# Kernel tuning notes

Measured on AMD Instinct MI355X. Metric: run time of the kernel, lower is better.

Reference implementation:

```python
import jax, jax.numpy as jnp
import numpy as np

N_NODES = 50000
N_EDGES = 800000
N_REL = 16
D = 64          # entity_dim == relation_dim == n_hidden
NEG_SLOPE = 0.01  # torch F.leaky_relu default


def setup_inputs() -> dict:
    key = jax.random.key(0)
    ks = jax.random.split(key, 12)
    s = 1.0 / np.sqrt(D)
    return {
        "node_ids": jnp.arange(N_NODES, dtype=jnp.int64) if jax.config.jax_enable_x64 else jnp.arange(N_NODES, dtype=jnp.int32),
        "relation_ids": jax.random.randint(ks[0], (N_EDGES,), 0, N_REL),
        "src": jax.random.randint(ks[1], (N_EDGES,), 0, N_NODES),
        "dst": jax.random.randint(ks[2], (N_EDGES,), 0, N_NODES),
        "entity_embed": jax.random.normal(ks[3], (N_NODES, D), jnp.float32) * s,
        "relation_embed": jax.random.normal(ks[4], (N_REL, D), jnp.float32) * s,
        "W0": jax.random.normal(ks[5], (N_REL, D, D), jnp.float32) * s,
        "W1": jax.random.normal(ks[6], (N_REL, D, D), jnp.float32) * s,
        "ra0": jax.random.normal(ks[7], (D, D), jnp.float32) * s,
        "rb0": jax.random.normal(ks[8], (D, D), jnp.float32) * s,
        "ra1": jax.random.normal(ks[9], (D, D), jnp.float32) * s,
        "rb1": jax.random.normal(ks[10], (D, D), jnp.float32) * s,
    }


def _edge_softmax(scores, dst, n_nodes):
    # segment softmax over edges grouped by destination node (DGL edge_softmax)
    m = jax.ops.segment_max(scores, dst, num_segments=n_nodes)  # [N]
    e = jnp.exp(scores - m[dst])                                # [E]
    z = jax.ops.segment_sum(e, dst, num_segments=n_nodes)       # [N]
    return e / z[dst]


def _kgat_layer(h, efeat, src, dst, etype, Wr, ra, rb, n_nodes):
    # transform every node under every relation once: [N, R, Dr]
    trans = jnp.einsum('nd,rde->nre', h, Wr)
    t_r = trans[src, etype]                   # W_r h_t  [E, Dr]
    h_r = trans[dst, etype]                   # W_r h_h  [E, Dr]
    att = jnp.sum(t_r * jnp.tanh(h_r + efeat), axis=1)  # [E]
    a = _edge_softmax(att, dst, n_nodes)                 # [E]
    # u_mul_e + sum: scatter-add weighted source features to dst
    h_nb = jax.ops.segment_sum(h[src] * a[:, None], dst, num_segments=n_nodes)
    # Bi residual
    out = (jax.nn.leaky_relu((h + h_nb) @ ra, NEG_SLOPE)
           + jax.nn.leaky_relu((h * h_nb) @ rb, NEG_SLOPE))
    return out


def reference(node_ids, relation_ids, src, dst, entity_embed, relation_embed,
              W0, W1, ra0, rb0, ra1, rb1):
    h = entity_embed[node_ids]                 # [N, D]
    efeat = relation_embed[relation_ids]       # [E, D]
    n_nodes = node_ids.shape[0]
    cache = [h]
    for Wr, ra, rb in ((W0, ra0, rb0), (W1, ra1, rb1)):
        h = _kgat_layer(h, efeat, src, dst, relation_ids, Wr, ra, rb, n_nodes)
        cache.append(h)
    return jnp.concatenate(cache, axis=1)      # [N, 3*D]
```

## Files before the change

### kernel.cpp

```cpp
#include <hip/hip_runtime.h>
#include <hip/hip_bf16.h>
#include <math.h>

#define NN 50000
#define NE 800000
#define NR 16
#define DD 64
#define OSTRIDE 192
#define QSTRIDE 1032

typedef __attribute__((ext_vector_type(8))) short bf16x8;
typedef __attribute__((ext_vector_type(4))) float f32x4;

__device__ inline float tanh_fast(float x) {
    return 1.f - 2.f / (__expf(2.f * x) + 1.f);
}
__device__ inline unsigned short f2bf(float f) {
    unsigned u = __float_as_uint(f);
    return (unsigned short)((u + 0x7fffu + ((u >> 16) & 1u)) >> 16);
}
__device__ inline float bf2f(unsigned short s) {
    return __uint_as_float((unsigned)s << 16);
}

__global__ void k_deg(const int* __restrict__ dst, int* __restrict__ cnt) {
    for (int e = blockIdx.x * blockDim.x + threadIdx.x; e < NE;
         e += gridDim.x * blockDim.x)
        atomicAdd(&cnt[dst[e]], 1);
}

__global__ __launch_bounds__(256) void k_scan1(const int* __restrict__ cnt,
                                               int* __restrict__ rowptr,
                                               int* __restrict__ bsum) {
    __shared__ int sh[256];
    int b = blockIdx.x, t = threadIdx.x;
    int i = b * 256 + t;
    int v = (i < NN) ? cnt[i] : 0;
    sh[t] = v;
    __syncthreads();
    #pragma unroll
    for (int o = 1; o < 256; o <<= 1) {
        int u = (t >= o) ? sh[t - o] : 0;
        __syncthreads();
        sh[t] += u;
        __syncthreads();
    }
    if (i < NN) rowptr[i] = sh[t] - v;
    if (t == 255) bsum[b] = sh[255];
}

__global__ __launch_bounds__(256) void k_scan2(int* __restrict__ bsum, int nb) {
    __shared__ int sh[256];
    int t = threadIdx.x;
    int v = (t < nb) ? bsum[t] : 0;
    sh[t] = v;
    __syncthreads();
    #pragma unroll
    for (int o = 1; o < 256; o <<= 1) {
        int u = (t >= o) ? sh[t - o] : 0;
        __syncthreads();
        sh[t] += u;
        __syncthreads();
    }
    if (t < nb) bsum[t] = sh[t] - v;
}

__global__ __launch_bounds__(256) void k_scan3(int* __restrict__ rowptr,
                                               const int* __restrict__ bsum,
                                               int* __restrict__ cursor) {
    int b = blockIdx.x, t = threadIdx.x;
    int i = b * 256 + t;
    if (i < NN) {
        int v = rowptr[i] + bsum[b];
        rowptr[i] = v;
        cursor[i] = v;
    }
    if (i == 0) rowptr[NN] = NE;
}

__global__ void k_fill(const int* __restrict__ dst, const int* __restrict__ src,
                       const int* __restrict__ rel, int* __restrict__ cursor,
                       int* __restrict__ epack) {
    for (int e = blockIdx.x * blockDim.x + threadIdx.x; e < NE;
         e += gridDim.x * blockDim.x) {
        int pos = atomicAdd(&cursor[dst[e]], 1);
        epack[pos] = src[e] | (rel[e] << 16);
    }
}

__global__ void k_copy_h0(const int* __restrict__ node_ids,
                          const float* __restrict__ ent,
                          float* __restrict__ out,
                          unsigned short* __restrict__ hbf) {
    int i = blockIdx.x * blockDim.x + threadIdx.x;
    if (i >= NN * DD) return;
    int n = i >> 6, d = i & 63;
    float v = ent[(size_t)node_ids[n] * DD + d];
    out[(size_t)n * OSTRIDE + d] = v;
    hbf[(size_t)n * DD + d] = f2bf(v);
}

__global__ void k_wprep(const float* __restrict__ W, unsigned short* __restrict__ wbf,
                        unsigned short* __restrict__ wtbf) {
    int i = blockIdx.x * blockDim.x + threadIdx.x;
    if (i >= NR * DD * DD) return;
    int r = i >> 12, rem = i & 4095, d = rem >> 6, E = rem & 63;
    unsigned short v = f2bf(W[i]);
    wbf[i] = v;
    wtbf[(r << 12) | (E << 6) | d] = v;
}

__global__ __launch_bounds__(1024) void k_fused6(const unsigned short* __restrict__ hbf,
                                                 const unsigned short* __restrict__ wbf,
                                                 const unsigned short* __restrict__ wtbf,
                                                 const float* __restrict__ relE,
                                                 const int* __restrict__ rowptr,
                                                 const int* __restrict__ epack,
                                                 float* __restrict__ h_nb) {
    __shared__ __align__(16) unsigned short q_lds[16 * QSTRIDE];
    __shared__ __align__(16) unsigned short u_lds[16][16][72];
    int n0 = blockIdx.x * 16;
    int t  = threadIdx.x;
    int w  = t >> 6, l = t & 63;
    int l15 = l & 15, lg = l >> 4;
    int r = w;

    {
        int ar = n0 + l15; if (ar >= NN) ar = NN - 1;
        const unsigned short* ap = hbf + (size_t)ar * DD + lg * 8;
        bf16x8 a0 = *(const bf16x8*)ap;
        bf16x8 a1 = *(const bf16x8*)(ap + 32);

        f32x4 acc[4];
        #pragma unroll
        for (int nt = 0; nt < 4; ++nt) acc[nt] = (f32x4){0.f, 0.f, 0.f, 0.f};
        const unsigned short* wtr = wtbf + (r << 12);
        #pragma unroll
        for (int nt = 0; nt < 4; ++nt) {
            const unsigned short* bp = wtr + (nt * 16 + l15) * DD + lg * 8;
            bf16x8 b0 = *(const bf16x8*)bp;
            bf16x8 b1 = *(const bf16x8*)(bp + 32);
            acc[nt] = __builtin_amdgcn_mfma_f32_16x16x32_bf16(a0, b0, acc[nt], 0, 0, 0);
            acc[nt] = __builtin_amdgcn_mfma_f32_16x16x32_bf16(a1, b1, acc[nt], 0, 0, 0);
        }

        #pragma unroll
        for (int nt = 0; nt < 4; ++nt) {
            int E = nt * 16 + l15;
            float er = relE[r * DD + E];
            #pragma unroll
            for (int reg = 0; reg < 4; ++reg)
                u_lds[w][lg * 4 + reg][E] = f2bf(tanh_fast(acc[nt][reg] + er));
        }
        asm volatile("s_waitcnt lgkmcnt(0)" ::: "memory");

        const unsigned short* up = &u_lds[w][l15][lg * 8];
        bf16x8 u0 = *(const bf16x8*)up;
        bf16x8 u1 = *(const bf16x8*)(up + 32);

        f32x4 q4[4];
        #pragma unroll
        for (int nt = 0; nt < 4; ++nt) q4[nt] = (f32x4){0.f, 0.f, 0.f, 0.f};
        const unsigned short* wr = wbf + (r << 12);
        #pragma unroll
        for (int nt = 0; nt < 4; ++nt) {
            const unsigned short* bp = wr + (nt * 16 + l15) * DD + lg * 8;
            bf16x8 b0 = *(const bf16x8*)bp;
            bf16x8 b1 = *(const bf16x8*)(bp + 32);
            q4[nt] = __builtin_amdgcn_mfma_f32_16x16x32_bf16(u0, b0, q4[nt], 0, 0, 0);
            q4[nt] = __builtin_amdgcn_mfma_f32_16x16x32_bf16(u1, b1, q4[nt], 0, 0, 0);
        }

        #pragma unroll
        for (int reg = 0; reg < 4; ++reg) {
            unsigned short* qp = q_lds + (lg * 4 + reg) * QSTRIDE + r * 64 + l15;
            #pragma unroll
            for (int nt = 0; nt < 4; ++nt)
                qp[nt * 16] = f2bf(q4[nt][reg]);
        }
    }
    __syncthreads();

    int n = n0 + w;
    if (n >= NN) return;
    int lane = l;
    const unsigned short* ql = q_lds + w * QSTRIDE;
    int row0 = rowptr[n], deg = rowptr[n + 1] - row0;

    float m = -__builtin_inff(), zr = 0.f, acc = 0.f;
    bool s0 = lane & 1, s1 = lane & 2, s2 = lane & 4;

    int i = 0;
    for (; i + 8 <= deg; i += 8) {
        float v[8], hv[8];
        #pragma unroll
        for (int j = 0; j < 8; ++j) {
            int p = epack[row0 + i + j];
            int s = p & 0xffff, rr = p >> 16;
            hv[j] = bf2f(hbf[(size_t)s * DD + lane]);
            v[j]  = hv[j] * bf2f(ql[rr * DD + lane]);
        }
        float x0 = s0 ? v[1] : v[0], o0 = s0 ? v[0] : v[1];
        float x1 = s0 ? v[3] : v[2], o1 = s0 ? v[2] : v[3];
        float x2 = s0 ? v[5] : v[4], o2 = s0 ? v[4] : v[5];
        float x3 = s0 ? v[7] : v[6], o3 = s0 ? v[6] : v[7];
        x0 += __shfl_xor(o0, 1, 64);
        x1 += __shfl_xor(o1, 1, 64);
        x2 += __shfl_xor(o2, 1, 64);
        x3 += __shfl_xor(o3, 1, 64);
        float y0 = s1 ? x1 : x0, p0 = s1 ? x0 : x1;
        float y1 = s1 ? x3 : x2, p1 = s1 ? x2 : x3;
        y0 += __shfl_xor(p0, 2, 64);
        y1 += __shfl_xor(p1, 2, 64);
        float sj = s2 ? y1 : y0, q0 = s2 ? y0 : y1;
        sj += __shfl_xor(q0, 4, 64);
        sj += __shfl_xor(sj, 8, 64);
        sj += __shfl_xor(sj, 16, 64);
        sj += __shfl_xor(sj, 32, 64);

        float cm = sj;
        cm = fmaxf(cm, __shfl_xor(cm, 1, 64));
        cm = fmaxf(cm, __shfl_xor(cm, 2, 64));
        cm = fmaxf(cm, __shfl_xor(cm, 4, 64));
        float mn = fmaxf(m, cm);
        float sc = __expf(m - mn);
        float wgt = __expf(sj - mn);
        float zn = wgt;
        zn += __shfl_xor(zn, 1, 64);
        zn += __shfl_xor(zn, 2, 64);
        zn += __shfl_xor(zn, 4, 64);
        zr = zr * sc + zn;
        acc *= sc;
        #pragma unroll
        for (int j = 0; j < 8; ++j)
            acc += __shfl(wgt, j, 8) * hv[j];
        m = mn;
    }
    for (; i < deg; ++i) {
        int p = epack[row0 + i];
        int s = p & 0xffff, rr = p >> 16;
        float hsv = bf2f(hbf[(size_t)s * DD + lane]);
        float v = hsv * bf2f(ql[rr * DD + lane]);
        #pragma unroll
        for (int o = 32; o; o >>= 1) v += __shfl_xor(v, o, 64);
        float mn = fmaxf(m, v);
        float sc = __expf(m - mn);
        float wgt = __expf(v - mn);
        zr  = zr * sc + wgt;
        acc = acc * sc + wgt * hsv;
        m = mn;
    }
    h_nb[(size_t)n * DD + lane] = (deg > 0) ? acc / zr : 0.f;
}

__global__ __launch_bounds__(256) void k_out2(const float* __restrict__ h_nb,
                                              const float* __restrict__ ra,
                                              const float* __restrict__ rb,
                                              float* __restrict__ out,
                                              int off_in, int off_out,
                                              unsigned short* __restrict__ hbf) {
    __shared__ __align__(16) float v1s[64][68];
    __shared__ __align__(16) float v2s[64][68];
    __shared__ __align__(16) float ws[2][64][64];
    int t = threadIdx.x;
    int n0 = blockIdx.x * 64;

    for (int i = t; i < 1024; i += 256) {
        int ni = i >> 4, c4 = (i & 15) * 4;
        int n = n0 + ni;
        float4 hv = make_float4(0.f, 0.f, 0.f, 0.f);
        float4 nb = make_float4(0.f, 0.f, 0.f, 0.f);
        if (n < NN) {
            hv = *(const float4*)&out[(size_t)n * OSTRIDE + off_in + c4];
            nb = *(const float4*)&h_nb[(size_t)n * DD + c4];
        }
        v1s[c4 + 0][ni] = hv.x + nb.x;  v2s[c4 + 0][ni] = hv.x * nb.x;
        v1s[c4 + 1][ni] = hv.y + nb.y;  v2s[c4 + 1][ni] = hv.y * nb.y;
        v1s[c4 + 2][ni] = hv.z + nb.z;  v2s[c4 + 2][ni] = hv.z * nb.z;
        v1s[c4 + 3][ni] = hv.w + nb.w;  v2s[c4 + 3][ni] = hv.w * nb.w;
    }
    for (int i = t; i < 2048; i += 256) {
        const float* base = (i < 1024) ? ra : rb;
        int rem = i & 1023;
        float4 v = *(const float4*)&base[rem * 4];
        int k = rem >> 4, c4 = (rem & 15) * 4;
        *(float4*)&ws[i >> 10][k][c4] = v;
    }
    __syncthreads();

    int nd0 = (t >> 4) * 4;
    int c0  = (t & 15) * 4;
    float a1[4][4] = {}, a2[4][4] = {};
    #pragma unroll 8
    for (int k = 0; k < 64; ++k) {
        float4 h1 = *(const float4*)&v1s[k][nd0];
        float4 h2 = *(const float4*)&v2s[k][nd0];
        float4 wa = *(const float4*)&ws[0][k][c0];
        float4 wb = *(const float4*)&ws[1][k][c0];
        float x1[4] = {h1.x, h1.y, h1.z, h1.w};
        float x2[4] = {h2.x, h2.y, h2.z, h2.w};
        #pragma unroll
        for (int i = 0; i < 4; ++i) {
            a1[i][0] += x1[i] * wa.x; a1[i][1] += x1[i] * wa.y;
            a1[i][2] += x1[i] * wa.z; a1[i][3] += x1[i] * wa.w;
            a2[i][0] += x2[i] * wb.x; a2[i][1] += x2[i] * wb.y;
            a2[i][2] += x2[i] * wb.z; a2[i][3] += x2[i] * wb.w;
        }
    }
    #pragma unroll
    for (int i = 0; i < 4; ++i) {
        int n = n0 + nd0 + i;
        if (n >= NN) continue;
        float4 o;
        float* po = (float*)&o;
        #pragma unroll
        for (int j = 0; j < 4; ++j) {
            float u1 = a1[i][j], u2 = a2[i][j];
            u1 = u1 > 0.f ? u1 : 0.01f * u1;
            u2 = u2 > 0.f ? u2 : 0.01f * u2;
            po[j] = u1 + u2;
        }
        *(float4*)&out[(size_t)n * OSTRIDE + off_out + c0] = o;
        hbf[(size_t)n * DD + c0 + 0] = f2bf(o.x);
        hbf[(size_t)n * DD + c0 + 1] = f2bf(o.y);
        hbf[(size_t)n * DD + c0 + 2] = f2bf(o.z);
        hbf[(size_t)n * DD + c0 + 3] = f2bf(o.w);
    }
}

extern "C" void kernel_launch(void* const* d_in, const int* in_sizes, int n_in,
                              void* d_out, int out_size, void* d_ws, size_t ws_size,
                              hipStream_t stream) {
    const int*   node_ids = (const int*)d_in[0];
    const int*   rel_ids  = (const int*)d_in[1];
    const int*   src      = (const int*)d_in[2];
    const int*   dst      = (const int*)d_in[3];
    const float* ent      = (const float*)d_in[4];
    const float* relE     = (const float*)d_in[5];
    const float* W[2]  = {(const float*)d_in[6], (const float*)d_in[7]};
    const float* ra[2] = {(const float*)d_in[8], (const float*)d_in[10]};
    const float* rb[2] = {(const float*)d_in[9], (const float*)d_in[11]};
    float* out = (float*)d_out;

    const size_t hnb_bytes    = (size_t)NN * DD * sizeof(float);
    const size_t hbf_bytes    = (size_t)NN * DD * sizeof(short);
    const size_t wbf_bytes    = (size_t)NR * DD * DD * sizeof(short);
    const size_t epack_bytes  = (size_t)NE * sizeof(int);
    const size_t rowptr_bytes = (size_t)(NN + 1) * sizeof(int);
    const size_t cnt_bytes    = (size_t)NN * sizeof(int);
    const int    NB_SCAN      = (NN + 255) / 256;
    const size_t bsum_bytes   = (size_t)256 * sizeof(int);

    char* p = (char*)d_ws;
    float*          h_nb   = (float*)p;          p += hnb_bytes;
    unsigned short* hbf    = (unsigned short*)p; p += hbf_bytes;
    unsigned short* wbf    = (unsigned short*)p; p += wbf_bytes;
    unsigned short* wtbf   = (unsigned short*)p; p += wbf_bytes;
    int*            epack  = (int*)p;            p += epack_bytes;
    int*            rowptr = (int*)p;            p += rowptr_bytes;
    int*            cnt    = (int*)p;            p += cnt_bytes;
    int*            bsum   = (int*)p;            p += bsum_bytes;
    (void)ws_size;

    hipMemsetAsync(cnt, 0, cnt_bytes, stream);
    k_deg  <<<1024, 256, 0, stream>>>(dst, cnt);
    k_scan1<<<NB_SCAN, 256, 0, stream>>>(cnt, rowptr, bsum);
    k_scan2<<<1, 256, 0, stream>>>(bsum, NB_SCAN);
    k_scan3<<<NB_SCAN, 256, 0, stream>>>(rowptr, bsum, cnt);
    k_fill <<<1024, 256, 0, stream>>>(dst, src, rel_ids, cnt, epack);

    k_copy_h0<<<(NN * DD + 255) / 256, 256, 0, stream>>>(node_ids, ent, out, hbf);

    for (int L = 0; L < 2; ++L) {
        int off_in = L * DD;
        int off_out = (L + 1) * DD;

        k_wprep <<<(NR * DD * DD + 255) / 256, 256, 0, stream>>>(W[L], wbf, wtbf);
        k_fused6<<<(NN + 15) / 16, 1024, 0, stream>>>(hbf, wbf, wtbf, relE,
                                                      rowptr, epack, h_nb);
        k_out2  <<<(NN + 63) / 64, 256, 0, stream>>>(h_nb, ra[L], rb[L], out,
                                                     off_in, off_out, hbf);
    }
}
```

Baseline: 458.7 us.

## Process four edges per wavefront concurrently with per-group online softmax merge

The per-node edge aggregation loop now splits the 64-lane wavefront into four 16-lane groups. Each group handles one edge at a time with 4 features per lane, loaded as vectorized uint2 reads. Each group keeps its own online-softmax max, sum and accumulators, and these are merged across groups with cross-lane shuffles at the end. This replaces the earlier 8-edge batched scheme that relied on long shuffle-reduction chains. The aim is to shorten reduction latency and widen memory loads, at the cost of masked idle lanes when the degree is not a multiple of four.

```diff
diff --git a/kernel.cpp b/kernel.cpp
--- a/kernel.cpp
+++ b/kernel.cpp
@@ -110,7 +110,7 @@
     wtbf[(r << 12) | (E << 6) | d] = v;
 }
 
-__global__ __launch_bounds__(1024) void k_fused6(const unsigned short* __restrict__ hbf,
+__global__ __launch_bounds__(1024) void k_fused7(const unsigned short* __restrict__ hbf,
                                                  const unsigned short* __restrict__ wbf,
                                                  const unsigned short* __restrict__ wtbf,
                                                  const float* __restrict__ relE,
@@ -183,74 +183,63 @@
 
     int n = n0 + w;
     if (n >= NN) return;
-    int lane = l;
     const unsigned short* ql = q_lds + w * QSTRIDE;
-    int row0 = rowptr[n], deg = rowptr[n + 1] - row0;
-
-    float m = -__builtin_inff(), zr = 0.f, acc = 0.f;
-    bool s0 = lane & 1, s1 = lane & 2, s2 = lane & 4;
-
-    int i = 0;
-    for (; i + 8 <= deg; i += 8) {
-        float v[8], hv[8];
-        #pragma unroll
-        for (int j = 0; j < 8; ++j) {
-            int p = epack[row0 + i + j];
-            int s = p & 0xffff, rr = p >> 16;
-            hv[j] = bf2f(hbf[(size_t)s * DD + lane]);
-            v[j]  = hv[j] * bf2f(ql[rr * DD + lane]);
-        }
-        float x0 = s0 ? v[1] : v[0], o0 = s0 ? v[0] : v[1];
-        float x1 = s0 ? v[3] : v[2], o1 = s0 ? v[2] : v[3];
-        float x2 = s0 ? v[5] : v[4], o2 = s0 ? v[4] : v[5];
-        float x3 = s0 ? v[7] : v[6], o3 = s0 ? v[6] : v[7];
-        x0 += __shfl_xor(o0, 1, 64);
-        x1 += __shfl_xor(o1, 1, 64);
-        x2 += __shfl_xor(o2, 1, 64);
-        x3 += __shfl_xor(o3, 1, 64);
-        float y0 = s1 ? x1 : x0, p0 = s1 ? x0 : x1;
-        float y1 = s1 ? x3 : x2, p1 = s1 ? x2 : x3;
-        y0 += __shfl_xor(p0, 2, 64);
-        y1 += __shfl_xor(p1, 2, 64);
-        float sj = s2 ? y1 : y0, q0 = s2 ? y0 : y1;
-        sj += __shfl_xor(q0, 4, 64);
-        sj += __shfl_xor(sj, 8, 64);
-        sj += __shfl_xor(sj, 16, 64);
-        sj += __shfl_xor(sj, 32, 64);
-
-        float cm = sj;
-        cm = fmaxf(cm, __shfl_xor(cm, 1, 64));
-        cm = fmaxf(cm, __shfl_xor(cm, 2, 64));
-        cm = fmaxf(cm, __shfl_xor(cm, 4, 64));
-        float mn = fmaxf(m, cm);
-        float sc = __expf(m - mn);
-        float wgt = __expf(sj - mn);
-        float zn = wgt;
-        zn += __shfl_xor(zn, 1, 64);
-        zn += __shfl_xor(zn, 2, 64);
-        zn += __shfl_xor(zn, 4, 64);
-        zr = zr * sc + zn;
-        acc *= sc;
-        #pragma unroll
-        for (int j = 0; j < 8; ++j)
-            acc += __shfl(wgt, j, 8) * hv[j];
-        m = mn;
-    }
-    for (; i < deg; ++i) {
-        int p = epack[row0 + i];
+    int row0 = rowptr[n], row1 = rowptr[n + 1];
+    int deg = row1 - row0;
+    int g = lg;
+
+    const float NEGBIG = -1e30f;
+    float m = NEGBIG, zr = 0.f;
+    float a0 = 0.f, a1 = 0.f, a2 = 0.f, a3 = 0.f;
+
+    int steps = (deg + 3) >> 2;
+    for (int k = 0; k < steps; ++k) {
+        int idx = row0 + (k << 2) + g;
+        bool ok = idx < row1;
+        int p = epack[ok ? idx : row0];
         int s = p & 0xffff, rr = p >> 16;
-        float hsv = bf2f(hbf[(size_t)s * DD + lane]);
-        float v = hsv * bf2f(ql[rr * DD + lane]);
-        #pragma unroll
-        for (int o = 32; o; o >>= 1) v += __shfl_xor(v, o, 64);
+        uint2 hu = *(const uint2*)(hbf + ((size_t)s << 6) + (l15 << 2));
+        uint2 qu = *(const uint2*)(ql + rr * 64 + (l15 << 2));
+        float h0 = __uint_as_float(hu.x << 16);
+        float h1 = __uint_as_float(hu.x & 0xffff0000u);
+        float h2 = __uint_as_float(hu.y << 16);
+        float h3 = __uint_as_float(hu.y & 0xffff0000u);
+        float q0 = __uint_as_float(qu.x << 16);
+        float q1 = __uint_as_float(qu.x & 0xffff0000u);
+        float q2 = __uint_as_float(qu.y << 16);
+        float q3 = __uint_as_float(qu.y & 0xffff0000u);
+        float d = h0 * q0 + h1 * q1 + h2 * q2 + h3 * q3;
+        d += __shfl_xor(d, 1, 64);
+        d += __shfl_xor(d, 2, 64);
+        d += __shfl_xor(d, 4, 64);
+        d += __shfl_xor(d, 8, 64);
+        float v  = ok ? d : NEGBIG;
         float mn = fmaxf(m, v);
         float sc = __expf(m - mn);
-        float wgt = __expf(v - mn);
-        zr  = zr * sc + wgt;
-        acc = acc * sc + wgt * hsv;
+        float wg = ok ? __expf(v - mn) : 0.f;
+        zr = zr * sc + wg;
+        a0 = a0 * sc + wg * h0;
+        a1 = a1 * sc + wg * h1;
+        a2 = a2 * sc + wg * h2;
+        a3 = a3 * sc + wg * h3;
         m = mn;
     }
-    h_nb[(size_t)n * DD + lane] = (deg > 0) ? acc / zr : 0.f;
+
+    float mo = fmaxf(m, __shfl_xor(m, 16, 64));
+    float ms = fmaxf(mo, __shfl_xor(mo, 32, 64));
+    float scg = __expf(m - ms);
+    zr *= scg; a0 *= scg; a1 *= scg; a2 *= scg; a3 *= scg;
+    zr += __shfl_xor(zr, 16, 64); zr += __shfl_xor(zr, 32, 64);
+    a0 += __shfl_xor(a0, 16, 64); a0 += __shfl_xor(a0, 32, 64);
+    a1 += __shfl_xor(a1, 16, 64); a1 += __shfl_xor(a1, 32, 64);
+    a2 += __shfl_xor(a2, 16, 64); a2 += __shfl_xor(a2, 32, 64);
+    a3 += __shfl_xor(a3, 16, 64); a3 += __shfl_xor(a3, 32, 64);
+
+    if (g == 0) {
+        float inv = (deg > 0) ? 1.f / zr : 0.f;
+        float4 o = make_float4(a0 * inv, a1 * inv, a2 * inv, a3 * inv);
+        *(float4*)&h_nb[((size_t)n << 6) + (l15 << 2)] = o;
+    }
 }
 
 __global__ __launch_bounds__(256) void k_out2(const float* __restrict__ h_nb,
@@ -376,7 +365,7 @@
         int off_out = (L + 1) * DD;
 
         k_wprep <<<(NR * DD * DD + 255) / 256, 256, 0, stream>>>(W[L], wbf, wtbf);
-        k_fused6<<<(NN + 15) / 16, 1024, 0, stream>>>(hbf, wbf, wtbf, relE,
+        k_fused7<<<(NN + 15) / 16, 1024, 0, stream>>>(hbf, wbf, wtbf, relE,
                                                       rowptr, epack, h_nb);
         k_out2  <<<(NN + 63) / 64, 256, 0, stream>>>(h_nb, ra[L], rb[L], out,
                                                      off_in, off_out, hbf);
```

Measured after the change: 434.8 us. 5.2% less time.
